# Optimization experiments

Measured on AMD Instinct MI355X. Metric: run time of the kernel, lower is better.

The kernel has to match this reference:

```python
import jax, jax.numpy as jnp
import numpy as np

B, S, D_MODEL, D_ATTN = 4, 2048, 1024, 128


def setup_inputs() -> dict:
    key = jax.random.key(0)
    ks = jax.random.split(key, 6)
    x = jax.random.normal(ks[0], (B, S, D_MODEL), dtype=jnp.float32)
    cross = jax.random.normal(ks[1], (B, S, D_MODEL), dtype=jnp.float32)
    # nn.Linear default init scale ~ 1/sqrt(fan_in); weights stored [out, in]
    sc = 1.0 / np.sqrt(D_MODEL)
    Wq = jax.random.normal(ks[2], (D_ATTN, D_MODEL), dtype=jnp.float32) * sc
    Wk = jax.random.normal(ks[3], (D_ATTN, D_MODEL), dtype=jnp.float32) * sc
    Wv = jax.random.normal(ks[4], (D_MODEL, D_MODEL), dtype=jnp.float32) * sc
    mask = jax.random.randint(ks[5], (B, S), 0, 2).astype(jnp.int32)
    return {"x": x, "cross": cross, "Wq": Wq, "Wk": Wk, "Wv": Wv, "mask": mask}


def reference(x, cross, Wq, Wk, Wv, mask):
    # projections (Linear with no bias): y = x @ W.T
    q = x @ Wq.T            # [B,S,d_attn]
    k = cross @ Wk.T        # [B,S,d_attn]
    v = x @ Wv.T            # [B,S,d_model]  (original uses x for v, not cross)
    logits = jnp.einsum('bsd,btd->bst', q, k)  # [B,S,S]

    s = x.shape[1]
    neg_inf = jnp.asarray(-jnp.inf, logits.dtype)
    # cross_attention=True branch: keep where triu(ones, diag=1)==0 -> lower tri incl. diag
    causal_keep = jnp.tril(jnp.ones((s, s), dtype=bool))
    logits = jnp.where(causal_keep[None, :, :], logits, neg_inf)

    # padding mask: outer product + eye; keep where > 0
    m = mask.astype(logits.dtype)                      # [B,S]
    square = m[:, :, None] * m[:, None, :]             # [B,S,S]
    square = square + jnp.eye(s, dtype=logits.dtype)[None, :, :]
    logits = jnp.where(square > 0, logits, neg_inf)

    attn = jax.nn.softmax(logits / np.sqrt(Wq.shape[0]).astype(np.float32), axis=-1)
    return attn @ v  # [B,S,d_model]
```

## Files before the change

### kernel.cpp

```cpp
#include <hip/hip_runtime.h>
#include <stdint.h>

#define B_ 4
#define S_ 2048
#define DM_ 1024
#define DA_ 128
#define SCALE 0.08838834764831845f
#define MSHIFT 8.0f

typedef short bf16x8 __attribute__((ext_vector_type(8)));
typedef float f32x4 __attribute__((ext_vector_type(4)));

__device__ __forceinline__ short f2bf(float f) {
  union { float f; unsigned u; } v; v.f = f;
  unsigned r = v.u + 0x7fffu + ((v.u >> 16) & 1u);
  return (short)(r >> 16);
}

__device__ __forceinline__ void gload16(const void* g, void* lds) {
  __builtin_amdgcn_global_load_lds(
      (const __attribute__((address_space(1))) unsigned int*)(uintptr_t)g,
      (__attribute__((address_space(3))) unsigned int*)(unsigned int)(uintptr_t)lds,
      16, 0, 0);
}

__global__ __launch_bounds__(256) void cvt_bulk(
    const float* __restrict__ x, short* __restrict__ xb,
    const float* __restrict__ cr, short* __restrict__ crb,
    const float* __restrict__ wv, short* __restrict__ wvb,
    const float* __restrict__ wq, short* __restrict__ wqb,
    const float* __restrict__ wk, short* __restrict__ wkb) {
  const int id = blockIdx.x;
  const float* s; short* d; int base;
  if (id < 8192)       { s = x;  d = xb;  base = id; }
  else if (id < 16384) { s = cr; d = crb; base = id - 8192; }
  else if (id < 17408) { s = wv; d = wvb; base = id - 16384; }
  else if (id < 17536) { s = wq; d = wqb; base = id - 17408; }
  else                 { s = wk; d = wkb; base = id - 17536; }
  const int i = base * 256 + threadIdx.x;
  float4 v = ((const float4*)s)[i];
  ((short4*)d)[i] = make_short4(f2bf(v.x), f2bf(v.y), f2bf(v.z), f2bf(v.w));
}

__global__ __launch_bounds__(128) void proj128(
    const short* __restrict__ xb, const short* __restrict__ crb,
    const short* __restrict__ Wvb, const short* __restrict__ Wqb,
    const short* __restrict__ Wkb,
    short* __restrict__ Qb, short* __restrict__ Kb, short* __restrict__ Vt) {
  __shared__ short As[2][128 * 32];
  __shared__ short Bs[2][128 * 32];
  const int id = blockIdx.x;
  const int tid = threadIdx.x;
  const int w = tid >> 6, lane = tid & 63;
  const int l15 = lane & 15, kq = lane >> 4;
  const int srow = tid >> 2;
  const int sch = ((tid & 3) ^ ((srow >> 1) & 3)) * 8;
  const int rch = (kq ^ ((l15 >> 1) & 3)) * 8;

  const short* gA;
  const short* gB;
  short* C; int ldc, m0, n0;
  if (id < 512) {
    const int x = id & 7, r = id >> 3;
    m0 = (r >> 3) * 128;
    n0 = (x * 8 + (r & 7)) * 128;
    gA = Wvb + (size_t)(m0 + srow) * DM_ + sch;
    gB = xb + (size_t)(n0 + srow) * DM_ + sch;
    C = Vt; ldc = B_ * S_;
  } else if (id < 576) {
    m0 = (id - 512) * 128; n0 = 0;
    gA = xb + (size_t)(m0 + srow) * DM_ + sch;
    gB = Wqb + (size_t)srow * DM_ + sch;
    C = Qb; ldc = DA_;
  } else {
    m0 = (id - 576) * 128; n0 = 0;
    gA = crb + (size_t)(m0 + srow) * DM_ + sch;
    gB = Wkb + (size_t)srow * DM_ + sch;
    C = Kb; ldc = DA_;
  }

#define STAGE_P(buf, kk)                                              \
  _Pragma("unroll")                                                   \
  for (int s = 0; s < 4; ++s) {                                       \
    gload16(gA + (kk) + (size_t)(s * 32) * DM_, &As[buf][s * 1024 + tid * 8]); \
    gload16(gB + (kk) + (size_t)(s * 32) * DM_, &Bs[buf][s * 1024 + tid * 8]); \
  }

  f32x4 acc[8][4] = {};
  STAGE_P(0, 0);
  __syncthreads();
  int cur = 0;
  for (int t = 0; t < 32; ++t) {
    const bool more = (t < 31);
    if (more) { STAGE_P(cur ^ 1, (t + 1) << 5); }
    bf16x8 af[8], bf[4];
#pragma unroll
    for (int q = 0; q < 8; ++q)
      af[q] = *(const bf16x8*)&As[cur][(q * 16 + l15) * 32 + rch];
#pragma unroll
    for (int q = 0; q < 4; ++q)
      bf[q] = *(const bf16x8*)&Bs[cur][(w * 64 + q * 16 + l15) * 32 + rch];
#pragma unroll
    for (int mt = 0; mt < 8; ++mt)
#pragma unroll
      for (int nt = 0; nt < 4; ++nt)
        acc[mt][nt] = __builtin_amdgcn_mfma_f32_16x16x32_bf16(af[mt], bf[nt], acc[mt][nt], 0, 0, 0);
    if (more) { __syncthreads(); cur ^= 1; }
  }
#undef STAGE_P
#pragma unroll
  for (int mt = 0; mt < 8; ++mt) {
    const int row = m0 + mt * 16 + kq * 4;
#pragma unroll
    for (int nt = 0; nt < 4; ++nt) {
      const int col = n0 + w * 64 + nt * 16 + l15;
#pragma unroll
      for (int r = 0; r < 4; ++r)
        C[(size_t)(row + r) * ldc + col] = f2bf(acc[mt][nt][r]);
    }
  }
}

__global__ __launch_bounds__(256) void pmat_kernel(
    const short* __restrict__ Q, const short* __restrict__ Kb,
    const int* __restrict__ mask, short* __restrict__ P) {
  __shared__ short Kls[64 * 128];
  const int bi = blockIdx.x;
  const int b = bi >> 5, it = bi & 31;
  const int jt = blockIdx.y;
  if (jt > it) return;
  const int i0 = it * 64, j0t = jt * 64;
  const int tid = threadIdx.x;
  const int wid = tid >> 6, lane = tid & 63;
  const int l15 = lane & 15, kofs = (lane >> 4) * 8, kq = lane >> 4;
  const int r0 = i0 + wid * 16;
  const size_t tokb = (size_t)b * S_;

  {
    const int srow16 = tid >> 4, c16 = tid & 15;
    const short* kg = Kb + (tokb + j0t + srow16) * DA_ + (c16 ^ (srow16 & 7)) * 8;
#pragma unroll
    for (int s = 0; s < 4; ++s)
      gload16(kg + (size_t)(s * 16) * DA_, &Kls[s * 2048 + tid * 8]);
  }

  bf16x8 qf[4];
  const short* qp = Q + (tokb + r0 + l15) * DA_ + kofs;
#pragma unroll
  for (int c = 0; c < 4; ++c) qf[c] = *(const bf16x8*)(qp + c * 32);
  const int lrow = wid * 16 + (lane >> 4) * 4;
  int mi[4];
#pragma unroll
  for (int r = 0; r < 4; ++r) mi[r] = mask[tokb + i0 + lrow + r];
  const size_t tbase = ((size_t)(b * 32 + it) * 64 + jt * 2) * 2048;
  __syncthreads();
#pragma unroll
  for (int ct = 0; ct < 4; ++ct) {
    f32x4 acc = {};
#pragma unroll
    for (int c = 0; c < 4; ++c) {
      const bf16x8 kf = *(const bf16x8*)&Kls[(ct * 16 + l15) * 128 +
                                            (((c * 4 + kq) ^ (l15 & 7)) * 8)];
      acc = __builtin_amdgcn_mfma_f32_16x16x32_bf16(qf[c], kf, acc, 0, 0, 0);
    }
    const int j = j0t + ct * 16 + l15;
    const int mj = mask[tokb + j];
    const size_t cbase = tbase + (size_t)(ct >> 1) * 2048 + (ct & 1) * 16 + l15;
#pragma unroll
    for (int r = 0; r < 4; ++r) {
      const int i = i0 + lrow + r;
      const bool keep = (j <= i) && (((mi[r] & mj) != 0) || (j == i));
      const float p = keep ? __expf(acc[r] * SCALE - MSHIFT) : 0.f;
      P[cbase + (lrow + r) * 32] = f2bf(p);
    }
  }
}

__global__ __launch_bounds__(256) void pv_gemm(
    const short* __restrict__ P, const short* __restrict__ Vt,
    float* __restrict__ O) {
  __shared__ short As[2][64 * 32];
  __shared__ short Bs[2][64 * 32];
  const int id = blockIdx.x;
  const int rem = id >> 3;
  const int g = 31 - (rem >> 3);
  const int b = (rem >> 1) & 3;
  const int vc = (id & 7) * 2 + (rem & 1);
  const int tokb = b * S_;
  const int m0 = tokb + g * 64;
  const int n0 = vc * 64;
  const int NT = (g + 1) * 2;
  const int tid = threadIdx.x;
  const int wid = tid >> 6, lane = tid & 63;
  const int l15 = lane & 15, kq = lane >> 4;
  const int srow = tid >> 2;
  const int sch = ((tid & 3) ^ ((srow >> 1) & 3)) * 8;
  const int rch = (kq ^ ((l15 >> 1) & 3)) * 8;
  const int wr = wid >> 1, wc = wid & 1;

  const short* ga = P + ((size_t)(b * 32 + g) * 64) * 2048 + srow * 32 + sch;
  const short* gb = Vt + (size_t)(n0 + srow) * (B_ * S_) + tokb + sch;

  const bf16x8 ones = {16256, 16256, 16256, 16256, 16256, 16256, 16256, 16256};

#define STAGE_PV(buf, t)                                 \
  gload16(ga + (size_t)(t) * 2048, &As[buf][tid * 8]);   \
  gload16(gb + ((t) << 5), &Bs[buf][tid * 8]);

  f32x4 acc[2][2] = {};
  f32x4 accl[2] = {};
  STAGE_PV(0, 0);
  __syncthreads();
  int cur = 0;
  for (int t = 0; t < NT; ++t) {
    if (t + 1 < NT) { STAGE_PV(cur ^ 1, t + 1); }
    bf16x8 af[2], bf[2];
#pragma unroll
    for (int q = 0; q < 2; ++q) {
      af[q] = *(const bf16x8*)&As[cur][(wr * 32 + q * 16 + l15) * 32 + rch];
      bf[q] = *(const bf16x8*)&Bs[cur][(wc * 32 + q * 16 + l15) * 32 + rch];
    }
#pragma unroll
    for (int mt = 0; mt < 2; ++mt) {
#pragma unroll
      for (int nt = 0; nt < 2; ++nt)
        acc[mt][nt] = __builtin_amdgcn_mfma_f32_16x16x32_bf16(af[mt], bf[nt], acc[mt][nt], 0, 0, 0);
      accl[mt] = __builtin_amdgcn_mfma_f32_16x16x32_bf16(af[mt], ones, accl[mt], 0, 0, 0);
    }
    if (t + 1 < NT) { __syncthreads(); cur ^= 1; }
  }
#undef STAGE_PV
#pragma unroll
  for (int mt = 0; mt < 2; ++mt) {
    const int row = m0 + wr * 32 + mt * 16 + kq * 4;
#pragma unroll
    for (int r = 0; r < 4; ++r) {
      const float inv = 1.0f / accl[mt][r];
#pragma unroll
      for (int nt = 0; nt < 2; ++nt) {
        const int col = n0 + wc * 32 + nt * 16 + l15;
        O[(size_t)(row + r) * DM_ + col] = acc[mt][nt][r] * inv;
      }
    }
  }
}

extern "C" void kernel_launch(void* const* d_in, const int* in_sizes, int n_in,
                              void* d_out, int out_size, void* d_ws, size_t ws_size,
                              hipStream_t stream) {
  const float* x  = (const float*)d_in[0];
  const float* cr = (const float*)d_in[1];
  const float* Wq = (const float*)d_in[2];
  const float* Wk = (const float*)d_in[3];
  const float* Wv = (const float*)d_in[4];
  const int* mask = (const int*)d_in[5];
  float* out = (float*)d_out;
  char* ws = (char*)d_ws;
  const size_t MiB = 1u << 20;
  short* xb  = (short*)(ws);
  short* crb = (short*)(ws + 16 * MiB);
  short* Pb  = (short*)(ws);
  short* Wvb = (short*)(ws + 32 * MiB);
  short* Vt  = (short*)(ws + 34 * MiB);
  short* Qb  = (short*)(ws + 50 * MiB);
  short* Kb  = (short*)(ws + 52 * MiB);
  short* Wqb = (short*)(ws + 54 * MiB);
  short* Wkb = (short*)(ws + 54 * MiB + 256 * 1024);

  cvt_bulk<<<17664, 256, 0, stream>>>(x, xb, cr, crb, Wv, Wvb, Wq, Wqb, Wk, Wkb);
  proj128<<<640, 128, 0, stream>>>(xb, crb, Wvb, Wqb, Wkb, Qb, Kb, Vt);
  pmat_kernel<<<dim3(128, 32), 256, 0, stream>>>(Qb, Kb, mask, Pb);
  pv_gemm<<<2048, 256, 0, stream>>>(Pb, Vt, out);
}
```

Measured before the change: 113.2 us.

## Fuse fp32-to-bf16 activation conversion into projection GEMM loads

The separate bulk conversion of x and cross to bf16 is removed. The projection kernel now reads fp32 activations directly, converts them in registers and writes them swizzled into LDS, so the bf16 copies are never written to or read back from global memory. The block is also widened from 2 to 4 waves, each owning a 64x64 sub-tile, which lowers accumulator registers per thread. In exchange the activation loads go through registers instead of direct-to-LDS, which costs VGPRs and may reduce the overlap of loads with compute.

```diff
diff --git a/kernel.cpp b/kernel.cpp
--- a/kernel.cpp
+++ b/kernel.cpp
@@ -17,6 +17,13 @@
   return (short)(r >> 16);
 }
 
+__device__ __forceinline__ bf16x8 cvt8(const float4 a, const float4 b) {
+  bf16x8 o;
+  o[0] = f2bf(a.x); o[1] = f2bf(a.y); o[2] = f2bf(a.z); o[3] = f2bf(a.w);
+  o[4] = f2bf(b.x); o[5] = f2bf(b.y); o[6] = f2bf(b.z); o[7] = f2bf(b.w);
+  return o;
+}
+
 __device__ __forceinline__ void gload16(const void* g, void* lds) {
   __builtin_amdgcn_global_load_lds(
       (const __attribute__((address_space(1))) unsigned int*)(uintptr_t)g,
@@ -24,96 +31,125 @@
       16, 0, 0);
 }
 
-__global__ __launch_bounds__(256) void cvt_bulk(
-    const float* __restrict__ x, short* __restrict__ xb,
-    const float* __restrict__ cr, short* __restrict__ crb,
+__global__ __launch_bounds__(256) void cvt_w(
     const float* __restrict__ wv, short* __restrict__ wvb,
     const float* __restrict__ wq, short* __restrict__ wqb,
     const float* __restrict__ wk, short* __restrict__ wkb) {
   const int id = blockIdx.x;
   const float* s; short* d; int base;
-  if (id < 8192)       { s = x;  d = xb;  base = id; }
-  else if (id < 16384) { s = cr; d = crb; base = id - 8192; }
-  else if (id < 17408) { s = wv; d = wvb; base = id - 16384; }
-  else if (id < 17536) { s = wq; d = wqb; base = id - 17408; }
-  else                 { s = wk; d = wkb; base = id - 17536; }
+  if (id < 1024)      { s = wv; d = wvb; base = id; }
+  else if (id < 1152) { s = wq; d = wqb; base = id - 1024; }
+  else                { s = wk; d = wkb; base = id - 1152; }
   const int i = base * 256 + threadIdx.x;
   float4 v = ((const float4*)s)[i];
   ((short4*)d)[i] = make_short4(f2bf(v.x), f2bf(v.y), f2bf(v.z), f2bf(v.w));
 }
 
-__global__ __launch_bounds__(128) void proj128(
-    const short* __restrict__ xb, const short* __restrict__ crb,
+__global__ __launch_bounds__(256) void proj128(
+    const float* __restrict__ x, const float* __restrict__ cr,
     const short* __restrict__ Wvb, const short* __restrict__ Wqb,
     const short* __restrict__ Wkb,
     short* __restrict__ Qb, short* __restrict__ Kb, short* __restrict__ Vt) {
-  __shared__ short As[2][128 * 32];
-  __shared__ short Bs[2][128 * 32];
+  __shared__ short Gs[2][128 * 32];
+  __shared__ short Ss[2][128 * 32];
   const int id = blockIdx.x;
   const int tid = threadIdx.x;
-  const int w = tid >> 6, lane = tid & 63;
+  const int wid = tid >> 6, lane = tid & 63;
   const int l15 = lane & 15, kq = lane >> 4;
-  const int srow = tid >> 2;
+  const int wr = wid >> 1, wc = wid & 1;
+  const int srow = (tid >> 2) & 63;
   const int sch = ((tid & 3) ^ ((srow >> 1) & 3)) * 8;
+  const int fr = tid >> 1, fh = tid & 1;
+  const int fch0 = ((fh * 2 + 0) ^ ((fr >> 1) & 3)) * 8;
+  const int fch1 = ((fh * 2 + 1) ^ ((fr >> 1) & 3)) * 8;
   const int rch = (kq ^ ((l15 >> 1) & 3)) * 8;
 
-  const short* gA;
-  const short* gB;
-  short* C; int ldc, m0, n0;
+  const short* gG;
+  const float* gF;
+  short* C; int ldc, m0, n0; bool gIsM;
   if (id < 512) {
-    const int x = id & 7, r = id >> 3;
+    const int xx = id & 7, r = id >> 3;
     m0 = (r >> 3) * 128;
-    n0 = (x * 8 + (r & 7)) * 128;
-    gA = Wvb + (size_t)(m0 + srow) * DM_ + sch;
-    gB = xb + (size_t)(n0 + srow) * DM_ + sch;
-    C = Vt; ldc = B_ * S_;
+    n0 = (xx * 8 + (r & 7)) * 128;
+    gG = Wvb + (size_t)(m0 + srow) * DM_ + sch;
+    gF = x + (size_t)(n0 + fr) * DM_ + fh * 16;
+    C = Vt; ldc = B_ * S_; gIsM = true;
   } else if (id < 576) {
     m0 = (id - 512) * 128; n0 = 0;
-    gA = xb + (size_t)(m0 + srow) * DM_ + sch;
-    gB = Wqb + (size_t)srow * DM_ + sch;
-    C = Qb; ldc = DA_;
+    gG = Wqb + (size_t)srow * DM_ + sch;
+    gF = x + (size_t)(m0 + fr) * DM_ + fh * 16;
+    C = Qb; ldc = DA_; gIsM = false;
   } else {
     m0 = (id - 576) * 128; n0 = 0;
-    gA = crb + (size_t)(m0 + srow) * DM_ + sch;
-    gB = Wkb + (size_t)srow * DM_ + sch;
-    C = Kb; ldc = DA_;
-  }
-
-#define STAGE_P(buf, kk)                                              \
-  _Pragma("unroll")                                                   \
-  for (int s = 0; s < 4; ++s) {                                       \
-    gload16(gA + (kk) + (size_t)(s * 32) * DM_, &As[buf][s * 1024 + tid * 8]); \
-    gload16(gB + (kk) + (size_t)(s * 32) * DM_, &Bs[buf][s * 1024 + tid * 8]); \
-  }
-
-  f32x4 acc[8][4] = {};
-  STAGE_P(0, 0);
+    gG = Wkb + (size_t)srow * DM_ + sch;
+    gF = cr + (size_t)(m0 + fr) * DM_ + fh * 16;
+    C = Kb; ldc = DA_; gIsM = false;
+  }
+  const int gsel = gIsM ? wr : wc;
+  const int ssel = gIsM ? wc : wr;
+
+#define GSTAGE(buf, kk)                                             \
+  gload16(gG + (kk), &Gs[buf][srow * 32 + sch]);                    \
+  gload16(gG + (kk) + (size_t)64 * DM_, &Gs[buf][(srow + 64) * 32 + sch]);
+#define FLOAD(kk)                                                   \
+  pa = *(const float4*)(gF + (kk)); pb = *(const float4*)(gF + (kk) + 4); \
+  pc = *(const float4*)(gF + (kk) + 8); pd = *(const float4*)(gF + (kk) + 12);
+#define FWRITE(buf)                                                 \
+  *(bf16x8*)&Ss[buf][fr * 32 + fch0] = cvt8(pa, pb);                \
+  *(bf16x8*)&Ss[buf][fr * 32 + fch1] = cvt8(pc, pd);
+#define COMPUTE(buf)                                                         \
+  {                                                                          \
+    bf16x8 fG[4], fS[4];                                                     \
+    _Pragma("unroll")                                                        \
+    for (int q = 0; q < 4; ++q) {                                            \
+      fG[q] = *(const bf16x8*)&Gs[buf][(gsel * 64 + q * 16 + l15) * 32 + rch]; \
+      fS[q] = *(const bf16x8*)&Ss[buf][(ssel * 64 + q * 16 + l15) * 32 + rch]; \
+    }                                                                        \
+    if (gIsM) {                                                              \
+      _Pragma("unroll")                                                      \
+      for (int mt = 0; mt < 4; ++mt)                                         \
+        _Pragma("unroll")                                                    \
+        for (int nt = 0; nt < 4; ++nt)                                       \
+          acc[mt][nt] = __builtin_amdgcn_mfma_f32_16x16x32_bf16(             \
+              fG[mt], fS[nt], acc[mt][nt], 0, 0, 0);                         \
+    } else {                                                                 \
+      _Pragma("unroll")                                                      \
+      for (int mt = 0; mt < 4; ++mt)                                         \
+        _Pragma("unroll")                                                    \
+        for (int nt = 0; nt < 4; ++nt)                                       \
+          acc[mt][nt] = __builtin_amdgcn_mfma_f32_16x16x32_bf16(             \
+              fS[mt], fG[nt], acc[mt][nt], 0, 0, 0);                         \
+    }                                                                        \
+  }
+
+  f32x4 acc[4][4] = {};
+  float4 pa, pb, pc, pd;
+  FLOAD(0);
+  GSTAGE(0, 0);
+  FWRITE(0);
   __syncthreads();
   int cur = 0;
   for (int t = 0; t < 32; ++t) {
     const bool more = (t < 31);
-    if (more) { STAGE_P(cur ^ 1, (t + 1) << 5); }
-    bf16x8 af[8], bf[4];
-#pragma unroll
-    for (int q = 0; q < 8; ++q)
-      af[q] = *(const bf16x8*)&As[cur][(q * 16 + l15) * 32 + rch];
-#pragma unroll
-    for (int q = 0; q < 4; ++q)
-      bf[q] = *(const bf16x8*)&Bs[cur][(w * 64 + q * 16 + l15) * 32 + rch];
-#pragma unroll
-    for (int mt = 0; mt < 8; ++mt)
-#pragma unroll
-      for (int nt = 0; nt < 4; ++nt)
-        acc[mt][nt] = __builtin_amdgcn_mfma_f32_16x16x32_bf16(af[mt], bf[nt], acc[mt][nt], 0, 0, 0);
-    if (more) { __syncthreads(); cur ^= 1; }
-  }
-#undef STAGE_P
-#pragma unroll
-  for (int mt = 0; mt < 8; ++mt) {
-    const int row = m0 + mt * 16 + kq * 4;
+    const int kk = (t + 1) << 5;
+    if (more) { FLOAD(kk); GSTAGE(cur ^ 1, kk); }
+    COMPUTE(cur);
+    if (more) {
+      FWRITE(cur ^ 1);
+      __syncthreads();
+      cur ^= 1;
+    }
+  }
+#undef GSTAGE
+#undef FLOAD
+#undef FWRITE
+#undef COMPUTE
+#pragma unroll
+  for (int mt = 0; mt < 4; ++mt) {
+    const int row = m0 + wr * 64 + mt * 16 + kq * 4;
 #pragma unroll
     for (int nt = 0; nt < 4; ++nt) {
-      const int col = n0 + w * 64 + nt * 16 + l15;
+      const int col = n0 + wc * 64 + nt * 16 + l15;
 #pragma unroll
       for (int r = 0; r < 4; ++r)
         C[(size_t)(row + r) * ldc + col] = f2bf(acc[mt][nt][r]);
@@ -257,8 +293,6 @@
   float* out = (float*)d_out;
   char* ws = (char*)d_ws;
   const size_t MiB = 1u << 20;
-  short* xb  = (short*)(ws);
-  short* crb = (short*)(ws + 16 * MiB);
   short* Pb  = (short*)(ws);
   short* Wvb = (short*)(ws + 32 * MiB);
   short* Vt  = (short*)(ws + 34 * MiB);
@@ -267,8 +301,8 @@
   short* Wqb = (short*)(ws + 54 * MiB);
   short* Wkb = (short*)(ws + 54 * MiB + 256 * 1024);
 
-  cvt_bulk<<<17664, 256, 0, stream>>>(x, xb, cr, crb, Wv, Wvb, Wq, Wqb, Wk, Wkb);
-  proj128<<<640, 128, 0, stream>>>(xb, crb, Wvb, Wqb, Wkb, Qb, Kb, Vt);
+  cvt_w<<<1280, 256, 0, stream>>>(Wv, Wvb, Wq, Wqb, Wk, Wkb);
+  proj128<<<640, 256, 0, stream>>>(x, cr, Wvb, Wqb, Wkb, Qb, Kb, Vt);
   pmat_kernel<<<dim3(128, 32), 256, 0, stream>>>(Qb, Kb, mask, Pb);
   pv_gemm<<<2048, 256, 0, stream>>>(Pb, Vt, out);
 }
```

Measured after the change: 124.1 us. 9.6% more time.
